# Kernel optimization log

Measured on AMD Instinct MI355X. Metric: run time of the kernel, lower is better.

Reference implementation:

```python
import jax, jax.numpy as jnp
import numpy as np

B, S, HID = 2, 2048, 4096
NH, NKV, HD = 32, 8, 128
MAX_POS = 4096
SCALE = HD ** -0.5


def _rope_tables():
    inv_freq = 1.0 / (10000.0 ** (np.arange(0, HD, 2, dtype=np.float32) / HD))
    t = np.arange(MAX_POS, dtype=np.float32)
    freqs = np.outer(t, inv_freq)              # [MAX_POS, HD/2]
    emb = np.concatenate([freqs, freqs], axis=-1)  # [MAX_POS, HD]
    return jnp.asarray(np.cos(emb)), jnp.asarray(np.sin(emb))


def setup_inputs() -> dict:
    key = jax.random.key(0)
    ks = jax.random.split(key, 6)
    hidden_states = jax.random.normal(ks[0], (B, S, HID), dtype=jnp.float32)
    position_ids = jnp.broadcast_to(jnp.arange(S, dtype=jnp.int64 if jax.config.jax_enable_x64 else jnp.int32), (B, S))
    cos_table, sin_table = _rope_tables()
    # weights stored [in, out] for x @ W
    sd = HID ** -0.5
    Wq = jax.random.normal(ks[1], (HID, NH * HD), dtype=jnp.float32) * sd
    Wk = jax.random.normal(ks[2], (HID, NKV * HD), dtype=jnp.float32) * sd
    Wv = jax.random.normal(ks[3], (HID, NKV * HD), dtype=jnp.float32) * sd
    Wo = jax.random.normal(ks[4], (NH * HD, HID), dtype=jnp.float32) * sd
    return {"hidden_states": hidden_states, "position_ids": position_ids,
            "cos_table": cos_table, "sin_table": sin_table,
            "Wq": Wq, "Wk": Wk, "Wv": Wv, "Wo": Wo}


def _rotate_half(x):
    x1, x2 = jnp.split(x, 2, axis=-1)
    return jnp.concatenate([-x2, x1], axis=-1)


def reference(hidden_states, position_ids, cos_table, sin_table, Wq, Wk, Wv, Wo):
    b, s, _ = hidden_states.shape
    q = (hidden_states @ Wq).reshape(b, s, NH, HD)
    k = (hidden_states @ Wk).reshape(b, s, NKV, HD)
    v = (hidden_states @ Wv).reshape(b, s, NKV, HD)

    # RoPE, cos/sin gathered by position and unsqueezed at head dim (dim=2, bsnd)
    cos = cos_table[position_ids][:, :, None, :]  # [b, s, 1, hd]
    sin = sin_table[position_ids][:, :, None, :]
    q = q * cos + _rotate_half(q) * sin
    k = k * cos + _rotate_half(k) * sin

    # GQA: expand kv heads to match query heads
    rep = NH // NKV
    k = jnp.repeat(k, rep, axis=2)  # [b, s, NH, hd]
    v = jnp.repeat(v, rep, axis=2)

    scores = jnp.einsum('bqnd,bknd->bnqk', q, k) * SCALE  # [b, NH, s, s]
    causal = jnp.tril(jnp.ones((s, s), dtype=bool))
    scores = jnp.where(causal, scores, jnp.finfo(scores.dtype).min)
    probs = jax.nn.softmax(scores, axis=-1)
    attn = jnp.einsum('bnqk,bknd->bqnd', probs, v)  # [b, s, NH, hd]
    attn = attn.reshape(b, s, NH * HD)
    return attn @ Wo
```

## Files before the change

kernel.cpp:

```cpp
#include <hip/hip_runtime.h>
#include <stdint.h>

typedef unsigned short u16;
typedef __bf16 bf16x8 __attribute__((ext_vector_type(8)));
typedef unsigned short u16x8 __attribute__((ext_vector_type(8)));
typedef unsigned short u16x4 __attribute__((ext_vector_type(4)));
typedef float f32x4 __attribute__((ext_vector_type(4)));

#define B_ 2
#define S_ 2048
#define HID_ 4096
#define NH_ 32
#define NKV_ 8
#define HD_ 128
#define NTOT_ 6144
#define SCALE_ 0.08838834764831845f

#define GLD16(gp, lp)                                                     \
  __builtin_amdgcn_global_load_lds(                                       \
      (__attribute__((address_space(1))) void*)(gp),                      \
      (__attribute__((address_space(3))) void*)(lp), 16, 0, 0)

#define BAR __builtin_amdgcn_s_barrier()
#define PRIO1 __builtin_amdgcn_s_setprio(1)
#define PRIO0 __builtin_amdgcn_s_setprio(0)
#define VM4 asm volatile("s_waitcnt vmcnt(4)" ::: "memory")
#define VM0 asm volatile("s_waitcnt vmcnt(0)" ::: "memory")

__device__ __forceinline__ u16 f2b(float f) {
  union { float f; uint32_t u; } v; v.f = f;
  uint32_t u = v.u;
  u = u + 0x7fffu + ((u >> 16) & 1u);
  return (u16)(u >> 16);
}
__device__ __forceinline__ float b2f(u16 s) {
  union { uint32_t u; float f; } v; v.u = ((uint32_t)s) << 16;
  return v.f;
}
__device__ __forceinline__ bf16x8 ldb8(const u16* p) {
  u16x8 u = *(const u16x8*)p;
  return __builtin_bit_cast(bf16x8, u);
}
__device__ __forceinline__ bf16x8 ldb8b(const char* p) {
  u16x8 u = *(const u16x8*)p;
  return __builtin_bit_cast(bf16x8, u);
}

__global__ __launch_bounds__(256) void k_convx(const float* __restrict__ src,
                                               u16* __restrict__ dst, int n4) {
  int i = blockIdx.x * 256 + threadIdx.x;
  if (i >= n4) return;
  const float4 v = ((const float4*)src)[i];
  u16x4 o = { f2b(v.x), f2b(v.y), f2b(v.z), f2b(v.w) };
  *(u16x4*)(dst + (size_t)i * 4) = o;
}

__global__ __launch_bounds__(256) void k_convT(const float* __restrict__ src,
                                               u16* __restrict__ dst, int N, int Kd) {
  __shared__ u16 tile[64][65];
  int k0 = blockIdx.x * 64, n0 = blockIdx.y * 64;
  int t = threadIdx.x;
  int rr = t >> 4;
  int cc = (t & 15) * 4;
#pragma unroll
  for (int p = 0; p < 4; ++p) {
    int r = p * 16 + rr;
    float4 v = *(const float4*)&src[(size_t)(k0 + r) * N + n0 + cc];
    tile[cc + 0][r] = f2b(v.x);
    tile[cc + 1][r] = f2b(v.y);
    tile[cc + 2][r] = f2b(v.z);
    tile[cc + 3][r] = f2b(v.w);
  }
  __syncthreads();
#pragma unroll
  for (int p = 0; p < 4; ++p) {
    int n = p * 16 + rr;
    u16x4 o = { tile[n][cc], tile[n][cc + 1], tile[n][cc + 2], tile[n][cc + 3] };
    *(u16x4*)&dst[(size_t)(n0 + n) * Kd + k0 + cc] = o;
  }
}

__global__ __launch_bounds__(512) void k_gemm_out(const u16* __restrict__ A,
                                                  const u16* __restrict__ Bt,
                                                  float* __restrict__ Cf,
                                                  int M, int N, int Kd) {
  __shared__ __align__(16) char smem[131072];
  const int NT = Kd >> 6;

  int nwg = gridDim.x * gridDim.y;
  int orig = blockIdx.y * gridDim.x + blockIdx.x;
  int cpx = nwg >> 3;
  int swz = (orig & 7) * cpx + (orig >> 3);
  int bx = swz % gridDim.x, by = swz / gridDim.x;
  int m0 = by * 256, n0 = bx * 256;

  int t = threadIdx.x, lane = t & 63, wave = t >> 6;
  int wr = wave >> 2, wc = wave & 3;
  int lg = lane >> 4, l16 = lane & 15;
  int loff = l16 * 64 + ((lg ^ ((l16 >> 1) & 3)) << 4);
  int srow = lane >> 2, schk = (lane & 3) ^ ((lane >> 3) & 3);

  const u16* Asrc = A  + (size_t)(m0 + wave * 32 + srow) * Kd + schk * 8;
  const u16* Bsrc = Bt + (size_t)(n0 + wave * 32 + srow) * Kd + schk * 8;

  f32x4 acc[8][4] = {};

#define OST_A(tile, kc, BB) do {                                              \
    char* d_ = smem + (BB) + ((kc) << 14) + (wave << 11);                     \
    const u16* s_ = Asrc + (size_t)(tile) * 64 + (kc) * 32;                   \
    GLD16(s_, d_); GLD16(s_ + (size_t)16 * Kd, d_ + 1024); } while (0)
#define OST_B(tile, kc, BB) do {                                              \
    char* d_ = smem + (BB) + 32768 + ((kc) << 14) + (wave << 11);             \
    const u16* s_ = Bsrc + (size_t)(tile) * 64 + (kc) * 32;                   \
    GLD16(s_, d_); GLD16(s_ + (size_t)16 * Kd, d_ + 1024); } while (0)

#define OPH(BB, kc, tl, OB, DS) do {                                          \
    bf16x8 bfr[4], af0[4], af1[4];                                            \
    _Pragma("unroll")                                                         \
    for (int j = 0; j < 4; ++j)                                               \
      bfr[j] = ldb8b(smem + (BB) + 32768 + ((kc) << 14) + ((wc * 4 + j) << 10) + loff); \
    _Pragma("unroll")                                                         \
    for (int i = 0; i < 4; ++i)                                               \
      af0[i] = ldb8b(smem + (BB) + ((kc) << 14) + ((wr * 8 + i) << 10) + loff); \
    _Pragma("unroll")                                                         \
    for (int i = 0; i < 4; ++i)                                               \
      af1[i] = ldb8b(smem + (BB) + ((kc) << 14) + ((wr * 8 + 4 + i) << 10) + loff); \
    if (DS) { OST_A(tl, kc, OB); OST_B(tl, kc, OB); VM4; } else { VM0; }      \
    BAR; PRIO1;                                                               \
    _Pragma("unroll")                                                         \
    for (int i = 0; i < 4; ++i) { _Pragma("unroll")                           \
      for (int j = 0; j < 4; ++j)                                             \
        acc[i][j] = __builtin_amdgcn_mfma_f32_16x16x32_bf16(af0[i], bfr[j], acc[i][j], 0, 0, 0); } \
    _Pragma("unroll")                                                         \
    for (int i = 0; i < 4; ++i) { _Pragma("unroll")                           \
      for (int j = 0; j < 4; ++j)                                             \
        acc[4 + i][j] = __builtin_amdgcn_mfma_f32_16x16x32_bf16(af1[i], bfr[j], acc[4 + i][j], 0, 0, 0); } \
    PRIO0; } while (0)

  OST_A(0, 0, 0); OST_B(0, 0, 0); OST_A(0, 1, 0); OST_B(0, 1, 0);
  VM4; BAR;

  for (int it = 0; it < (NT >> 1); ++it) {
    int a = it << 1;
    bool pf = (a + 2 < NT);
    OPH(0,     0, a + 1, 65536, true);
    OPH(0,     1, a + 1, 65536, true);
    OPH(65536, 0, a + 2, 0,     pf);
    OPH(65536, 1, a + 2, 0,     pf);
  }
#undef OPH
#undef OST_A
#undef OST_B

#pragma unroll
  for (int i = 0; i < 8; ++i)
#pragma unroll
    for (int j = 0; j < 4; ++j)
#pragma unroll
      for (int r = 0; r < 4; ++r) {
        int m = m0 + wr * 128 + i * 16 + lg * 4 + r;
        int n = n0 + wc * 64 + j * 16 + l16;
        Cf[(size_t)m * N + n] = acc[i][j][r];
      }
}

__global__ __launch_bounds__(512) void k_gqkv(const u16* __restrict__ A,
                                              const u16* __restrict__ Bt,
                                              u16* __restrict__ Qb,
                                              u16* __restrict__ Kb,
                                              u16* __restrict__ Vb) {
  __shared__ __align__(16) char smem[114688];
  const int Kd = HID_;
  const int NT = Kd >> 6;

  int orig = blockIdx.y * 32 + blockIdx.x;
  int swz = (orig & 7) * 64 + (orig >> 3);
  int bx = swz & 31, by = swz >> 5;
  int m0 = by * 256, n0 = bx * 192;

  int t = threadIdx.x, lane = t & 63, wave = t >> 6;
  int wr = wave >> 2, wc = wave & 3;
  int lg = lane >> 4, l16 = lane & 15;
  int loff = l16 * 64 + ((lg ^ ((l16 >> 1) & 3)) << 4);
  int srow = lane >> 2, schk = (lane & 3) ^ ((lane >> 3) & 3);

  const u16* Asrc = A + (size_t)(m0 + wave * 32 + srow) * Kd + schk * 8;
  const u16* sB0 = Bt + (size_t)(n0 + wave * 16 + srow) * Kd + schk * 8;
  const u16* sB1 = Bt + (size_t)(n0 + 128 + (wave & 3) * 16 + srow) * Kd + schk * 8;
  int bdst2 = (8 + (wave & 3)) << 10;

  f32x4 acc[8][3] = {};

#define QST_A(tile, kc, BB) do {                                              \
    char* d_ = smem + (BB) + ((kc) << 14) + (wave << 11);                     \
    const u16* s_ = Asrc + (size_t)(tile) * 64 + (kc) * 32;                   \
    GLD16(s_, d_); GLD16(s_ + (size_t)16 * Kd, d_ + 1024); } while (0)
#define QST_B(tile, kc, BB) do {                                              \
    char* db_ = smem + (BB) + 32768 + (kc) * 12288;                           \
    GLD16(sB0 + (size_t)(tile) * 64 + (kc) * 32, db_ + (wave << 10));         \
    GLD16(sB1 + (size_t)(tile) * 64 + (kc) * 32, db_ + bdst2); } while (0)

#define QPH(BB, kc, tl, OB, DS) do {                                          \
    bf16x8 bfr[3], af0[4], af1[4];                                            \
    _Pragma("unroll")                                                         \
    for (int j = 0; j < 3; ++j)                                               \
      bfr[j] = ldb8b(smem + (BB) + 32768 + (kc) * 12288 + ((wc * 3 + j) << 10) + loff); \
    _Pragma("unroll")                                                         \
    for (int i = 0; i < 4; ++i)                                               \
      af0[i] = ldb8b(smem + (BB) + ((kc) << 14) + ((wr * 8 + i) << 10) + loff); \
    _Pragma("unroll")                                                         \
    for (int i = 0; i < 4; ++i)                                               \
      af1[i] = ldb8b(smem + (BB) + ((kc) << 14) + ((wr * 8 + 4 + i) << 10) + loff); \
    if (DS) { QST_A(tl, kc, OB); QST_B(tl, kc, OB); VM4; } else { VM0; }      \
    BAR; PRIO1;                                                               \
    _Pragma("unroll")                                                         \
    for (int i = 0; i < 4; ++i) { _Pragma("unroll")                           \
      for (int j = 0; j < 3; ++j)                                             \
        acc[i][j] = __builtin_amdgcn_mfma_f32_16x16x32_bf16(af0[i], bfr[j], acc[i][j], 0, 0, 0); } \
    _Pragma("unroll")                                                         \
    for (int i = 0; i < 4; ++i) { _Pragma("unroll")                           \
      for (int j = 0; j < 3; ++j)                                             \
        acc[4 + i][j] = __builtin_amdgcn_mfma_f32_16x16x32_bf16(af1[i], bfr[j], acc[4 + i][j], 0, 0, 0); } \
    PRIO0; } while (0)

  QST_A(0, 0, 0); QST_B(0, 0, 0); QST_A(0, 1, 0); QST_B(0, 1, 0);
  VM4; BAR;

  for (int it = 0; it < (NT >> 1); ++it) {
    int a = it << 1;
    bool pf = (a + 2 < NT);
    QPH(0,     0, a + 1, 57344, true);
    QPH(0,     1, a + 1, 57344, true);
    QPH(57344, 0, a + 2, 0,     pf);
    QPH(57344, 1, a + 2, 0,     pf);
  }
#undef QPH
#undef QST_A
#undef QST_B

#pragma unroll
  for (int i = 0; i < 8; ++i)
#pragma unroll
    for (int j = 0; j < 3; ++j)
#pragma unroll
      for (int r = 0; r < 4; ++r) {
        int m = m0 + wr * 128 + i * 16 + lg * 4 + r;
        int n = n0 + wc * 48 + j * 16 + l16;
        int head = n >> 7, d = n & 127;
        int b = m >> 11, s = m & (S_ - 1);
        u16 val = f2b(acc[i][j][r]);
        if (head < NH_) {
          Qb[(((size_t)b * NH_ + head) * S_ + s) * HD_ + d] = val;
        } else if (head < NH_ + NKV_) {
          Kb[(((size_t)b * NKV_ + (head - NH_)) * S_ + s) * HD_ + d] = val;
        } else {
          Vb[(((size_t)b * NKV_ + (head - NH_ - NKV_)) * HD_ + d) * S_ + s] = val;
        }
      }
}

__global__ __launch_bounds__(256) void k_rope(u16* __restrict__ buf, const int* __restrict__ pos,
                                              const float* __restrict__ ct, const float* __restrict__ st,
                                              int H, int rows) {
  int wave = threadIdx.x >> 6, lane = threadIdx.x & 63;
  int row = blockIdx.x * 4 + wave;
  if (row >= rows) return;
  int s = row & (S_ - 1);
  int b = row / (H * S_);
  int p = pos[b * S_ + s];
  size_t base = (size_t)row * HD_;
  float x1 = b2f(buf[base + lane]);
  float x2 = b2f(buf[base + 64 + lane]);
  float c  = ct[(size_t)p * HD_ + lane];
  float sn = st[(size_t)p * HD_ + lane];
  buf[base + lane]      = f2b(x1 * c - x2 * sn);
  buf[base + 64 + lane] = f2b(x2 * c + x1 * sn);
}

__global__ __launch_bounds__(256, 4) void k_attn(const u16* __restrict__ Q,
                                                 const u16* __restrict__ K,
                                                 const u16* __restrict__ Vt,
                                                 u16* __restrict__ Ob) {
  __shared__ __align__(16) char smem[40960];
  const int VS_OFF = 16384, PS_OFF = 32768;

  int bid = blockIdx.x;
  int pid = bid & 15;
  int h   = (bid >> 4) & 31;
  int b   = bid >> 9;
  int kvh = h >> 2;
  int tid = threadIdx.x;
  int wave = tid >> 6, lane = tid & 63;
  int lg = lane >> 4, l16 = lane & 15;
  int lsw = (l16 & 7) << 4;

  const u16* Qp = Q  + (((size_t)b * NH_  + h)   * S_) * HD_;
  const u16* Kp = K  + (((size_t)b * NKV_ + kvh) * S_) * HD_;
  const u16* Vp = Vt + (((size_t)b * NKV_ + kvh) * HD_) * S_;

  for (int pass = 0; pass < 2; ++pass) {
    int qt = pass ? (31 - pid) : pid;
    int q0 = qt * 64 + wave * 16;
    int qg = q0 + l16;

    bf16x8 qf[4];
#pragma unroll
    for (int c = 0; c < 4; ++c)
      qf[c] = ldb8(&Qp[(size_t)qg * HD_ + c * 32 + lg * 8]);

    f32x4 oacc[8] = {};
    float mrun = -1e30f, lrun = 0.f;

    int nt = qt + 1;
    for (int tI = 0; tI < nt; ++tI) {
      int kb = tI * 64;
      __syncthreads();
#pragma unroll
      for (int i = 0; i < 4; ++i) {
        int ci = i * 256 + tid;
        int r = ci >> 4, ch = ci & 15;
        u16x8 v = *(const u16x8*)&Kp[(size_t)(kb + r) * HD_ + ch * 8];
        *(u16x8*)(smem + r * 256 + ((ch * 16) ^ ((r & 7) << 4))) = v;
      }
#pragma unroll
      for (int i = 0; i < 4; ++i) {
        int ci = i * 256 + tid;
        int r = ci >> 3, ch = ci & 7;
        u16x8 v = *(const u16x8*)&Vp[(size_t)r * S_ + kb + ch * 8];
        *(u16x8*)(smem + VS_OFF + r * 128 + ((ch * 16) ^ ((r & 7) << 4))) = v;
      }
      __syncthreads();

      f32x4 sc[4] = {};
#pragma unroll
      for (int c = 0; c < 4; ++c) {
#pragma unroll
        for (int n = 0; n < 4; ++n) {
          bf16x8 kf = ldb8b(smem + (n * 16 + l16) * 256 + ((c * 64 + lg * 16) ^ lsw));
          sc[n] = __builtin_amdgcn_mfma_f32_16x16x32_bf16(kf, qf[c], sc[n], 0, 0, 0);
        }
      }

      bool diag = (tI == qt);
      float mx = -1e30f;
#pragma unroll
      for (int n = 0; n < 4; ++n)
#pragma unroll
        for (int r = 0; r < 4; ++r) {
          float v = sc[n][r];
          int key = kb + n * 16 + lg * 4 + r;
          if (diag && key > qg) v = -1e30f;
          sc[n][r] = v;
          mx = fmaxf(mx, v);
        }
      mx = fmaxf(mx, __shfl_xor(mx, 16));
      mx = fmaxf(mx, __shfl_xor(mx, 32));
      float mnew = fmaxf(mrun, mx * SCALE_);
      float alpha = __expf(mrun - mnew);
      float ps = 0.f;
#pragma unroll
      for (int n = 0; n < 4; ++n) {
        u16x4 pk;
#pragma unroll
        for (int r = 0; r < 4; ++r) {
          float p = __expf(fmaf(sc[n][r], SCALE_, -mnew));
          ps += p;
          pk[r] = f2b(p);
        }
        *(u16x4*)(smem + PS_OFF + wave * 2048 + l16 * 128 + ((n * 32 + lg * 8) ^ lsw)) = pk;
      }
      ps += __shfl_xor(ps, 16);
      ps += __shfl_xor(ps, 32);
      lrun = lrun * alpha + ps;
      mrun = mnew;

      float ar[4];
#pragma unroll
      for (int r = 0; r < 4; ++r) ar[r] = __shfl(alpha, lg * 4 + r);
#pragma unroll
      for (int ns = 0; ns < 8; ++ns)
#pragma unroll
        for (int r = 0; r < 4; ++r) oacc[ns][r] *= ar[r];

#pragma unroll
      for (int ck = 0; ck < 2; ++ck) {
        bf16x8 pa = ldb8b(smem + PS_OFF + wave * 2048 + l16 * 128 + ((ck * 64 + lg * 16) ^ lsw));
#pragma unroll
        for (int ns = 0; ns < 8; ++ns) {
          bf16x8 vf = ldb8b(smem + VS_OFF + (ns * 16 + l16) * 128 + ((ck * 64 + lg * 16) ^ lsw));
          oacc[ns] = __builtin_amdgcn_mfma_f32_16x16x32_bf16(pa, vf, oacc[ns], 0, 0, 0);
        }
      }
    }

    float lr[4];
#pragma unroll
    for (int r = 0; r < 4; ++r) lr[r] = 1.0f / __shfl(lrun, lg * 4 + r);
#pragma unroll
    for (int ns = 0; ns < 8; ++ns)
#pragma unroll
      for (int r = 0; r < 4; ++r) {
        int q = q0 + lg * 4 + r;
        Ob[((size_t)(b * S_) + q) * (NH_ * HD_) + h * HD_ + ns * 16 + l16] =
            f2b(oacc[ns][r] * lr[r]);
      }
  }
}

extern "C" void kernel_launch(void* const* d_in, const int* in_sizes, int n_in,
                              void* d_out, int out_size, void* d_ws, size_t ws_size,
                              hipStream_t stream) {
  const float* hs  = (const float*)d_in[0];
  const int*   pos = (const int*)d_in[1];
  const float* ct  = (const float*)d_in[2];
  const float* st  = (const float*)d_in[3];
  const float* Wq  = (const float*)d_in[4];
  const float* Wk  = (const float*)d_in[5];
  const float* Wv  = (const float*)d_in[6];
  const float* Wo  = (const float*)d_in[7];
  float* out = (float*)d_out;

  char* w = (char*)d_ws;
  u16* Xb    = (u16*)(w);
  u16* WqkvT = (u16*)(w + 33554432ull);
  u16* WoT   = (u16*)(w + 83886080ull);
  u16* Qb    = (u16*)(w + 117440512ull);
  u16* Kb    = (u16*)(w + 150994944ull);
  u16* Vb    = (u16*)(w + 159383552ull);
  u16* Attb  = (u16*)(w + 167772160ull);

  k_convx<<<16384, 256, 0, stream>>>(hs, Xb, 4194304);
  k_convT<<<dim3(64, 64), 256, 0, stream>>>(Wq, WqkvT, 4096, 4096);
  k_convT<<<dim3(64, 16), 256, 0, stream>>>(Wk, WqkvT + (size_t)4096 * 4096, 1024, 4096);
  k_convT<<<dim3(64, 16), 256, 0, stream>>>(Wv, WqkvT + (size_t)5120 * 4096, 1024, 4096);
  k_convT<<<dim3(64, 64), 256, 0, stream>>>(Wo, WoT, 4096, 4096);
  k_gqkv<<<dim3(32, 16), 512, 0, stream>>>(Xb, WqkvT, Qb, Kb, Vb);
  k_rope<<<32768, 256, 0, stream>>>(Qb, pos, ct, st, NH_, B_ * NH_ * S_);
  k_rope<<<8192, 256, 0, stream>>>(Kb, pos, ct, st, NKV_, B_ * NKV_ * S_);
  k_attn<<<1024, 256, 0, stream>>>(Qb, Kb, Vb, Attb);
  k_gemm_out<<<dim3(16, 16), 512, 0, stream>>>(Attb, WoT, out, 4096, 4096, 4096);
}
```

Measured before the change: 617.5 us.

## Restructure GEMM pipelines to prefetch full next K-tile before compute

Both the output-projection GEMM and the fused QKV GEMM drop the half-tile interleaved prefetch schedule. They now use a simple per-K-tile double-buffer loop: issue all loads for the next tile, wait with vmcnt(8), barrier, run both k-chunks of MFMA, then barrier again. The aim is fewer barriers between halves and longer prefetch distance. In exchange, the LDS reads are no longer overlapped with issuing the global loads, a trailing barrier is added each iteration, and the buffer offsets become runtime values.

```diff
diff --git a/kernel.cpp b/kernel.cpp
--- a/kernel.cpp
+++ b/kernel.cpp
@@ -24,7 +24,7 @@
 #define BAR __builtin_amdgcn_s_barrier()
 #define PRIO1 __builtin_amdgcn_s_setprio(1)
 #define PRIO0 __builtin_amdgcn_s_setprio(0)
-#define VM4 asm volatile("s_waitcnt vmcnt(4)" ::: "memory")
+#define VM8 asm volatile("s_waitcnt vmcnt(8)" ::: "memory")
 #define VM0 asm volatile("s_waitcnt vmcnt(0)" ::: "memory")
 
 __device__ __forceinline__ u16 f2b(float f) {
@@ -113,8 +113,7 @@
     char* d_ = smem + (BB) + 32768 + ((kc) << 14) + (wave << 11);             \
     const u16* s_ = Bsrc + (size_t)(tile) * 64 + (kc) * 32;                   \
     GLD16(s_, d_); GLD16(s_ + (size_t)16 * Kd, d_ + 1024); } while (0)
-
-#define OPH(BB, kc, tl, OB, DS) do {                                          \
+#define OHALF(BB, kc) do {                                                    \
     bf16x8 bfr[4], af0[4], af1[4];                                            \
     _Pragma("unroll")                                                         \
     for (int j = 0; j < 4; ++j)                                               \
@@ -125,8 +124,7 @@
     _Pragma("unroll")                                                         \
     for (int i = 0; i < 4; ++i)                                               \
       af1[i] = ldb8b(smem + (BB) + ((kc) << 14) + ((wr * 8 + 4 + i) << 10) + loff); \
-    if (DS) { OST_A(tl, kc, OB); OST_B(tl, kc, OB); VM4; } else { VM0; }      \
-    BAR; PRIO1;                                                               \
+    PRIO1;                                                                    \
     _Pragma("unroll")                                                         \
     for (int i = 0; i < 4; ++i) { _Pragma("unroll")                           \
       for (int j = 0; j < 4; ++j)                                             \
@@ -138,17 +136,23 @@
     PRIO0; } while (0)
 
   OST_A(0, 0, 0); OST_B(0, 0, 0); OST_A(0, 1, 0); OST_B(0, 1, 0);
-  VM4; BAR;
-
-  for (int it = 0; it < (NT >> 1); ++it) {
-    int a = it << 1;
-    bool pf = (a + 2 < NT);
-    OPH(0,     0, a + 1, 65536, true);
-    OPH(0,     1, a + 1, 65536, true);
-    OPH(65536, 0, a + 2, 0,     pf);
-    OPH(65536, 1, a + 2, 0,     pf);
+
+  for (int kt = 0; kt < NT; ++kt) {
+    const int bb = (kt & 1) << 16;
+    const int ob = ((kt + 1) & 1) << 16;
+    if (kt + 1 < NT) {
+      OST_A(kt + 1, 0, ob); OST_B(kt + 1, 0, ob);
+      OST_A(kt + 1, 1, ob); OST_B(kt + 1, 1, ob);
+      VM8;
+    } else {
+      VM0;
+    }
+    BAR;
+    OHALF(bb, 0);
+    OHALF(bb, 1);
+    BAR;
   }
-#undef OPH
+#undef OHALF
 #undef OST_A
 #undef OST_B
 
@@ -199,8 +203,7 @@
     char* db_ = smem + (BB) + 32768 + (kc) * 12288;                           \
     GLD16(sB0 + (size_t)(tile) * 64 + (kc) * 32, db_ + (wave << 10));         \
     GLD16(sB1 + (size_t)(tile) * 64 + (kc) * 32, db_ + bdst2); } while (0)
-
-#define QPH(BB, kc, tl, OB, DS) do {                                          \
+#define QHALF(BB, kc) do {                                                    \
     bf16x8 bfr[3], af0[4], af1[4];                                            \
     _Pragma("unroll")                                                         \
     for (int j = 0; j < 3; ++j)                                               \
@@ -211,8 +214,7 @@
     _Pragma("unroll")                                                         \
     for (int i = 0; i < 4; ++i)                                               \
       af1[i] = ldb8b(smem + (BB) + ((kc) << 14) + ((wr * 8 + 4 + i) << 10) + loff); \
-    if (DS) { QST_A(tl, kc, OB); QST_B(tl, kc, OB); VM4; } else { VM0; }      \
-    BAR; PRIO1;                                                               \
+    PRIO1;                                                                    \
     _Pragma("unroll")                                                         \
     for (int i = 0; i < 4; ++i) { _Pragma("unroll")                           \
       for (int j = 0; j < 3; ++j)                                             \
@@ -224,17 +226,23 @@
     PRIO0; } while (0)
 
   QST_A(0, 0, 0); QST_B(0, 0, 0); QST_A(0, 1, 0); QST_B(0, 1, 0);
-  VM4; BAR;
-
-  for (int it = 0; it < (NT >> 1); ++it) {
-    int a = it << 1;
-    bool pf = (a + 2 < NT);
-    QPH(0,     0, a + 1, 57344, true);
-    QPH(0,     1, a + 1, 57344, true);
-    QPH(57344, 0, a + 2, 0,     pf);
-    QPH(57344, 1, a + 2, 0,     pf);
+
+  for (int kt = 0; kt < NT; ++kt) {
+    const int bb = (kt & 1) * 57344;
+    const int ob = ((kt + 1) & 1) * 57344;
+    if (kt + 1 < NT) {
+      QST_A(kt + 1, 0, ob); QST_B(kt + 1, 0, ob);
+      QST_A(kt + 1, 1, ob); QST_B(kt + 1, 1, ob);
+      VM8;
+    } else {
+      VM0;
+    }
+    BAR;
+    QHALF(bb, 0);
+    QHALF(bb, 1);
+    BAR;
   }
-#undef QPH
+#undef QHALF
 #undef QST_A
 #undef QST_B
 
```

Measured after the change: 698.4 us. 13.1% more time.
